# Kernel optimization log

Measured on AMD Instinct MI355X. Metric: run time of the kernel, lower is better.

The kernel has to match this reference:

```python
import jax, jax.numpy as jnp
import numpy as np

N_NODES = 50000
N_EDGES = 600000
D = 128


def _clip(x, c=1.0):
    # per-row L2 clip: x / max(||x|| / c, 1)
    n = jnp.linalg.norm(x, axis=-1, keepdims=True)
    return x / jnp.maximum(n / c, 1.0)


def _priv_sage_conv(x, edge_index, W, b, noise):
    # PrivSAGEConv.forward with perturbation_mode='aggr', root_weight=False
    xc = _clip(x, c=1.0)
    src, dst = edge_index[0], edge_index[1]
    # propagate: gather messages from source nodes, scatter-add at targets
    msg = jax.ops.segment_sum(xc[src], dst, num_segments=x.shape[0])  # [N, D]
    agg = xc + msg + noise  # self term + neighbor sum + DP noise
    return agg @ W.T + b


def setup_inputs() -> dict:
    key = jax.random.key(0)
    ks = jax.random.split(key, 8)
    x = jax.random.normal(ks[0], (N_NODES, D), dtype=jnp.float32)
    edge_index = jax.random.randint(ks[1], (2, N_EDGES), 0, N_NODES, dtype=jnp.int64)
    scale = 1.0 / np.sqrt(D)
    W1 = jax.random.normal(ks[2], (D, D), dtype=jnp.float32) * scale
    b1 = jnp.zeros((D,), dtype=jnp.float32)
    W2 = jax.random.normal(ks[3], (D, D), dtype=jnp.float32) * scale
    b2 = jnp.zeros((D,), dtype=jnp.float32)
    noise1 = jax.random.normal(ks[4], (N_NODES, D), dtype=jnp.float32)
    noise2 = jax.random.normal(ks[5], (N_NODES, D), dtype=jnp.float32)
    return {"x": x, "edge_index": edge_index, "W1": W1, "b1": b1,
            "W2": W2, "b2": b2, "noise1": noise1, "noise2": noise2}


def reference(x, edge_index, W1, b1, W2, b2, noise1, noise2):
    # Layer 1: conv -> (no batchnorm) -> dropout(identity, eval) -> SELU -> stack-combine
    h = _priv_sage_conv(x, edge_index, W1, b1, noise1)
    h = jax.nn.selu(h)
    # Layer 2: last layer, is_pred_module=True -> raw output
    out = _priv_sage_conv(h, edge_index, W2, b2, noise2)
    return out
```

## Files before the change

kernel.cpp:

```cpp
#include <hip/hip_runtime.h>

#define NN 50000
#define NE 600000
#define DD 128
#define NPAD 50048
#define SCAN_BLOCKS 49

typedef __attribute__((ext_vector_type(8))) short bf16x8;
typedef __attribute__((ext_vector_type(4))) float f32x4;

__device__ __forceinline__ float bf2f(unsigned int u16) {
    union { unsigned int i; float f; } v; v.i = u16 << 16; return v.f;
}
__device__ __forceinline__ unsigned short f2bf(float f) {
    union { float f; unsigned int i; } v; v.f = f;
    unsigned int i = v.i + 0x7FFFu + ((v.i >> 16) & 1u);
    return (unsigned short)(i >> 16);
}
__device__ __forceinline__ float wred64(float v) {
    #pragma unroll
    for (int o = 32; o; o >>= 1) v += __shfl_xor(v, o, 64);
    return v;
}
__device__ __forceinline__ int tame16(unsigned int u) {
    int e = (int)((u >> 7) & 0xFF);
    return (e >= 100 && e <= 133) ? 1 : 0;
}

__global__ void probe_k(const int* __restrict__ ei,
                        const unsigned int* __restrict__ xw,
                        const unsigned int* __restrict__ w1w,
                        const unsigned int* __restrict__ nzw,
                        int* __restrict__ flags) {
    const int lane = threadIdx.x;
    int nz = 0;
    #pragma unroll
    for (int i = 0; i < 4; ++i) nz |= ei[2 * (lane * 4 + i) + 1];
    int tx = tame16(xw[lane] & 0xFFFFu);
    int tw = tame16(w1w[lane] & 0xFFFFu);
    int tn = tame16(nzw[lane] & 0xFFFFu);
    #pragma unroll
    for (int o = 32; o; o >>= 1) {
        nz |= __shfl_xor(nz, o, 64);
        tx += __shfl_xor(tx, o, 64);
        tw += __shfl_xor(tw, o, 64);
        tn += __shfl_xor(tn, o, 64);
    }
    if (lane == 0) {
        flags[0] = (nz == 0) ? 1 : 0;
        flags[1] = (tx >= 48) ? 1 : 0;
        flags[2] = (tw >= 48) ? 1 : 0;
        flags[3] = (tn >= 48) ? 1 : 0;
    }
}

__global__ __launch_bounds__(256) void convert_k(
    const void* __restrict__ W1, const void* __restrict__ b1,
    const void* __restrict__ W2, const void* __restrict__ b2,
    const int* __restrict__ flags,
    unsigned short* __restrict__ W1b, unsigned short* __restrict__ b1b,
    unsigned short* __restrict__ W2b, unsigned short* __restrict__ b2b) {
    const int i = blockIdx.x * blockDim.x + threadIdx.x;
    if (i >= DD * DD) return;
    if (flags[2]) {
        W1b[i] = ((const unsigned short*)W1)[i];
        W2b[i] = ((const unsigned short*)W2)[i];
        if (i < DD) { b1b[i] = ((const unsigned short*)b1)[i];
                      b2b[i] = ((const unsigned short*)b2)[i]; }
    } else {
        W1b[i] = f2bf(((const float*)W1)[i]);
        W2b[i] = f2bf(((const float*)W2)[i]);
        if (i < DD) { b1b[i] = f2bf(((const float*)b1)[i]);
                      b2b[i] = f2bf(((const float*)b2)[i]); }
    }
}

__global__ __launch_bounds__(256) void hist_k(
    const int* __restrict__ ei, const int* __restrict__ flags,
    int* __restrict__ deg) {
    const int e = blockIdx.x * blockDim.x + threadIdx.x;
    if (e >= NE) return;
    const int d = flags[0] ? (int)((const long long*)ei)[NE + e] : ei[NE + e];
    atomicAdd(&deg[d], 1);
}

__global__ __launch_bounds__(1024) void scan1_k(
    const int* __restrict__ deg, int* __restrict__ offs,
    int* __restrict__ bsum) {
    __shared__ int wsum[16];
    __shared__ int wbase[16];
    __shared__ int tot_s;
    const int tid = threadIdx.x, lane = tid & 63, wv = tid >> 6;
    const int i = blockIdx.x * 1024 + tid;
    const int v = (i < NN) ? deg[i] : 0;
    int incl = v;
    #pragma unroll
    for (int off = 1; off < 64; off <<= 1) {
        int t = __shfl_up(incl, off, 64);
        if (lane >= off) incl += t;
    }
    if (lane == 63) wsum[wv] = incl;
    __syncthreads();
    if (wv == 0 && lane < 16) {
        const int wv_v = wsum[lane];
        int wincl = wv_v;
        #pragma unroll
        for (int off = 1; off < 16; off <<= 1) {
            int t = __shfl_up(wincl, off, 64);
            if (lane >= off) wincl += t;
        }
        wbase[lane] = wincl - wv_v;
        if (lane == 15) tot_s = wincl;
    }
    __syncthreads();
    if (i < NN) offs[i] = wbase[wv] + incl - v;
    if (tid == 0) bsum[blockIdx.x] = tot_s;
}

__global__ __launch_bounds__(1024) void scan2_k(
    int* __restrict__ offs, int* __restrict__ cursor,
    const int* __restrict__ bsum) {
    __shared__ int base_s;
    const int tid = threadIdx.x;
    if (tid < 64) {
        const int v = (tid < SCAN_BLOCKS) ? bsum[tid] : 0;
        int incl = v;
        #pragma unroll
        for (int off = 1; off < 64; off <<= 1) {
            int t = __shfl_up(incl, off, 64);
            if (tid >= off) incl += t;
        }
        if (tid == blockIdx.x) base_s = incl - v;
    }
    __syncthreads();
    const int i = blockIdx.x * 1024 + tid;
    if (i < NN) {
        const int o = offs[i] + base_s;
        offs[i] = o;
        cursor[i] = o;
    }
    if (blockIdx.x == 0 && tid == 0) offs[NN] = NE;
}

__global__ __launch_bounds__(256) void fill_k(
    const int* __restrict__ ei, const int* __restrict__ flags,
    int* __restrict__ cursor, int* __restrict__ eidx) {
    const int e = blockIdx.x * blockDim.x + threadIdx.x;
    if (e >= NE) return;
    int s, d;
    if (flags[0]) {
        const long long* e64 = (const long long*)ei;
        s = (int)e64[e]; d = (int)e64[NE + e];
    } else {
        s = ei[e]; d = ei[NE + e];
    }
    const int pos = atomicAdd(&cursor[d], 1);
    eidx[pos] = s;
}

__global__ __launch_bounds__(256) void prep_k(
    const void* __restrict__ x, const int* __restrict__ flags,
    unsigned int* __restrict__ featu) {
    const int row = (blockIdx.x * blockDim.x + threadIdx.x) >> 6;
    const int lane = threadIdx.x & 63;
    if (row >= NN) return;
    float v0, v1;
    if (flags[1]) {
        const unsigned int px = ((const unsigned int*)x)[(size_t)row * 64 + lane];
        v0 = bf2f(px & 0xFFFFu); v1 = bf2f(px >> 16);
    } else {
        const float2 px = ((const float2*)x)[(size_t)row * 64 + lane];
        v0 = px.x; v1 = px.y;
    }
    const float ss = wred64(v0 * v0 + v1 * v1);
    const float nrm = sqrtf(ss);
    const float sc = nrm > 1.0f ? 1.0f / nrm : 1.0f;
    featu[(size_t)row * 64 + lane] =
        (unsigned int)f2bf(v0 * sc) | ((unsigned int)f2bf(v1 * sc) << 16);
}

__global__ __launch_bounds__(256) void agg_k(
    const int* __restrict__ offs, const int* __restrict__ eidx,
    const unsigned int* __restrict__ featu, const void* __restrict__ noise,
    const int* __restrict__ flags, unsigned int* __restrict__ aggu) {
    const int node = (blockIdx.x * blockDim.x + threadIdx.x) >> 6;
    const int lane = threadIdx.x & 63;
    if (node >= NN) return;
    const unsigned int u0 = featu[(size_t)node * 64 + lane];
    float ax = bf2f(u0 & 0xFFFFu), ay = bf2f(u0 >> 16);
    if (flags[3]) {
        const unsigned int pn = ((const unsigned int*)noise)[(size_t)node * 64 + lane];
        ax += bf2f(pn & 0xFFFFu); ay += bf2f(pn >> 16);
    } else {
        const float2 n = ((const float2*)noise)[(size_t)node * 64 + lane];
        ax += n.x; ay += n.y;
    }
    const int e1 = offs[node + 1];
    int e = offs[node];
    for (; e + 7 < e1; e += 8) {
        int sidx[8];
        #pragma unroll
        for (int q = 0; q < 8; ++q) sidx[q] = eidx[e + q];
        unsigned int u[8];
        #pragma unroll
        for (int q = 0; q < 8; ++q) u[q] = featu[(size_t)sidx[q] * 64 + lane];
        #pragma unroll
        for (int q = 0; q < 8; ++q) {
            ax += bf2f(u[q] & 0xFFFFu);
            ay += bf2f(u[q] >> 16);
        }
    }
    for (; e < e1; ++e) {
        const unsigned int a = featu[(size_t)eidx[e] * 64 + lane];
        ax += bf2f(a & 0xFFFFu);
        ay += bf2f(a >> 16);
    }
    aggu[(size_t)node * 64 + lane] =
        (unsigned int)f2bf(ax) | ((unsigned int)f2bf(ay) << 16);
}

template<bool LAYER1>
__global__ __launch_bounds__(256) void gemm_k(
    const unsigned short* __restrict__ aggb,
    const unsigned short* __restrict__ Wb,
    const unsigned short* __restrict__ bb,
    unsigned short* __restrict__ featb,
    float* __restrict__ outf) {
    __shared__ unsigned short Wl[128 * 136];
    __shared__ unsigned short bl[128];
    const int t = threadIdx.x;
    #pragma unroll
    for (int i = 0; i < 8; ++i) {
        const int idx8 = t + i * 256;
        const int base = idx8 * 8;
        const int row = base >> 7, col = base & 127;
        *(uint4*)&Wl[row * 136 + col] = ((const uint4*)Wb)[idx8];
    }
    if (t < 128) bl[t] = bb[t];

    const int lane = t & 63;
    const int w = t >> 6;
    const int n15 = lane & 15;
    const int quad = lane >> 4;
    const int rbase = blockIdx.x * 64 + w * 16;

    bf16x8 af[4];
    #pragma unroll
    for (int kc = 0; kc < 4; ++kc)
        af[kc] = *(const bf16x8*)&aggb[(size_t)(rbase + n15) * DD + kc * 32 + quad * 8];

    __syncthreads();

    float h[32];
    #pragma unroll
    for (int nt = 0; nt < 8; ++nt) {
        f32x4 acc = {0.f, 0.f, 0.f, 0.f};
        #pragma unroll
        for (int kc = 0; kc < 4; ++kc) {
            const bf16x8 bfr =
                *(const bf16x8*)&Wl[(nt * 16 + n15) * 136 + kc * 32 + quad * 8];
            acc = __builtin_amdgcn_mfma_f32_16x16x32_bf16(af[kc], bfr, acc, 0, 0, 0);
        }
        const float bj = bf2f((unsigned int)bl[nt * 16 + n15]);
        #pragma unroll
        for (int r = 0; r < 4; ++r) h[nt * 4 + r] = acc[r] + bj;
    }

    if (LAYER1) {
        const float S = 1.0507009873554805f, AL = 1.6732632423543772f;
        float ss[4] = {0.f, 0.f, 0.f, 0.f};
        #pragma unroll
        for (int nt = 0; nt < 8; ++nt)
            #pragma unroll
            for (int r = 0; r < 4; ++r) {
                float v = h[nt * 4 + r];
                v = v > 0.f ? S * v : S * AL * expm1f(v);
                h[nt * 4 + r] = v;
                ss[r] += v * v;
            }
        #pragma unroll
        for (int r = 0; r < 4; ++r) {
            #pragma unroll
            for (int off = 1; off < 16; off <<= 1)
                ss[r] += __shfl_xor(ss[r], off, 64);
        }
        float sc[4];
        #pragma unroll
        for (int r = 0; r < 4; ++r) {
            const float nr = sqrtf(ss[r]);
            sc[r] = nr > 1.f ? 1.f / nr : 1.f;
        }
        #pragma unroll
        for (int r = 0; r < 4; ++r) {
            const int row = rbase + quad * 4 + r;
            if (row < NN) {
                #pragma unroll
                for (int nt = 0; nt < 8; ++nt)
                    featb[(size_t)row * DD + nt * 16 + n15] =
                        f2bf(h[nt * 4 + r] * sc[r]);
            }
        }
    } else {
        #pragma unroll
        for (int r = 0; r < 4; ++r) {
            const int row = rbase + quad * 4 + r;
            if (row < NN) {
                #pragma unroll
                for (int nt = 0; nt < 8; ++nt)
                    outf[(size_t)row * DD + nt * 16 + n15] = h[nt * 4 + r];
            }
        }
    }
}

extern "C" void kernel_launch(void* const* d_in, const int* in_sizes, int n_in,
                              void* d_out, int out_size, void* d_ws, size_t ws_size,
                              hipStream_t stream) {
    const void* x  = d_in[0];
    const int*  ei = (const int*)d_in[1];
    const void* W1 = d_in[2];
    const void* b1 = d_in[3];
    const void* W2 = d_in[4];
    const void* b2 = d_in[5];
    const void* n1 = d_in[6];
    const void* n2 = d_in[7];

    unsigned short* aggb = (unsigned short*)d_ws;
    unsigned short* W1b  = aggb + (size_t)NPAD * DD;
    unsigned short* b1b  = W1b + DD * DD;
    unsigned short* W2b  = b1b + DD;
    unsigned short* b2b  = W2b + DD * DD;
    int* flags  = (int*)(b2b + DD);
    int* deg    = flags + 4;
    int* offs   = deg + NN;
    int* cursor = offs + NN + 1;
    int* bsum   = cursor + NN;
    int* eidx   = bsum + 64;
    unsigned int* featu = (unsigned int*)d_out;

    probe_k<<<1, 64, 0, stream>>>(ei, (const unsigned int*)x,
                                  (const unsigned int*)W1,
                                  (const unsigned int*)n1, flags);
    convert_k<<<(DD * DD + 255) / 256, 256, 0, stream>>>(W1, b1, W2, b2, flags,
                                                         W1b, b1b, W2b, b2b);

    hipMemsetAsync(deg, 0, NN * sizeof(int), stream);
    hist_k<<<(NE + 255) / 256, 256, 0, stream>>>(ei, flags, deg);
    scan1_k<<<SCAN_BLOCKS, 1024, 0, stream>>>(deg, offs, bsum);
    scan2_k<<<SCAN_BLOCKS, 1024, 0, stream>>>(offs, cursor, bsum);
    fill_k<<<(NE + 255) / 256, 256, 0, stream>>>(ei, flags, cursor, eidx);

    prep_k<<<(NN * 64) / 256, 256, 0, stream>>>(x, flags, featu);
    agg_k<<<(NN * 64) / 256, 256, 0, stream>>>(offs, eidx, featu, n1, flags,
                                               (unsigned int*)aggb);
    gemm_k<true><<<NPAD / 64, 256, 0, stream>>>(aggb, W1b, b1b,
                                                (unsigned short*)featu, nullptr);

    agg_k<<<(NN * 64) / 256, 256, 0, stream>>>(offs, eidx, featu, n2, flags,
                                               (unsigned int*)aggb);
    gemm_k<false><<<NPAD / 64, 256, 0, stream>>>(aggb, W2b, b2b, nullptr,
                                                 (float*)d_out);
}
```

Measured before the change: 290.1 us.

## Split aggregation wavefront into half-waves gathering two edges with wider loads

```diff
diff --git a/kernel.cpp b/kernel.cpp
--- a/kernel.cpp
+++ b/kernel.cpp
@@ -163,7 +163,8 @@
     unsigned int* __restrict__ featu) {
     const int row = (blockIdx.x * blockDim.x + threadIdx.x) >> 6;
     const int lane = threadIdx.x & 63;
-    if (row >= NN) return;
+    if (row > NN) return;
+    if (row == NN) { featu[(size_t)NN * 64 + lane] = 0u; return; }
     float v0, v1;
     if (flags[1]) {
         const unsigned int px = ((const unsigned int*)x)[(size_t)row * 64 + lane];
@@ -181,42 +182,64 @@
 
 __global__ __launch_bounds__(256) void agg_k(
     const int* __restrict__ offs, const int* __restrict__ eidx,
-    const unsigned int* __restrict__ featu, const void* __restrict__ noise,
-    const int* __restrict__ flags, unsigned int* __restrict__ aggu) {
+    const uint2* __restrict__ featu2, const void* __restrict__ noise,
+    const int* __restrict__ flags, uint2* __restrict__ aggu2) {
     const int node = (blockIdx.x * blockDim.x + threadIdx.x) >> 6;
     const int lane = threadIdx.x & 63;
     if (node >= NN) return;
-    const unsigned int u0 = featu[(size_t)node * 64 + lane];
-    float ax = bf2f(u0 & 0xFFFFu), ay = bf2f(u0 >> 16);
-    if (flags[3]) {
-        const unsigned int pn = ((const unsigned int*)noise)[(size_t)node * 64 + lane];
-        ax += bf2f(pn & 0xFFFFu); ay += bf2f(pn >> 16);
-    } else {
-        const float2 n = ((const float2*)noise)[(size_t)node * 64 + lane];
-        ax += n.x; ay += n.y;
-    }
-    const int e1 = offs[node + 1];
-    int e = offs[node];
-    for (; e + 7 < e1; e += 8) {
-        int sidx[8];
-        #pragma unroll
-        for (int q = 0; q < 8; ++q) sidx[q] = eidx[e + q];
-        unsigned int u[8];
-        #pragma unroll
-        for (int q = 0; q < 8; ++q) u[q] = featu[(size_t)sidx[q] * 64 + lane];
-        #pragma unroll
-        for (int q = 0; q < 8; ++q) {
-            ax += bf2f(u[q] & 0xFFFFu);
-            ay += bf2f(u[q] >> 16);
-        }
-    }
-    for (; e < e1; ++e) {
-        const unsigned int a = featu[(size_t)eidx[e] * 64 + lane];
-        ax += bf2f(a & 0xFFFFu);
-        ay += bf2f(a >> 16);
-    }
-    aggu[(size_t)node * 64 + lane] =
-        (unsigned int)f2bf(ax) | ((unsigned int)f2bf(ay) << 16);
+    const int c = lane & 31;
+    const int h = lane >> 5;
+
+    float a0, a1, a2, a3;
+    if (h == 0) {
+        const uint2 s = featu2[(size_t)node * 32 + c];
+        a0 = bf2f(s.x & 0xFFFFu); a1 = bf2f(s.x >> 16);
+        a2 = bf2f(s.y & 0xFFFFu); a3 = bf2f(s.y >> 16);
+    } else {
+        if (flags[3]) {
+            const uint2 n = ((const uint2*)noise)[(size_t)node * 32 + c];
+            a0 = bf2f(n.x & 0xFFFFu); a1 = bf2f(n.x >> 16);
+            a2 = bf2f(n.y & 0xFFFFu); a3 = bf2f(n.y >> 16);
+        } else {
+            const float4 n = ((const float4*)noise)[(size_t)node * 32 + c];
+            a0 = n.x; a1 = n.y; a2 = n.z; a3 = n.w;
+        }
+    }
+
+    const int e0 = offs[node];
+    const int cnt = offs[node + 1] - e0;
+    for (int base = 0; base < cnt; base += 64) {
+        const int rem = cnt - base;
+        int myi = NN;
+        if (lane < rem) myi = eidx[e0 + base + lane];
+        const int pairs = (rem < 64 ? rem + 1 : 64) >> 1;
+        const int pb = (pairs + 7) & ~7;
+        for (int p = 0; p < pb; p += 8) {
+            uint2 u[8];
+            #pragma unroll
+            for (int q = 0; q < 8; ++q) {
+                const int s = __shfl(myi, 2 * (p + q) + h, 64);
+                u[q] = featu2[(size_t)s * 32 + c];
+            }
+            #pragma unroll
+            for (int q = 0; q < 8; ++q) {
+                a0 += bf2f(u[q].x & 0xFFFFu); a1 += bf2f(u[q].x >> 16);
+                a2 += bf2f(u[q].y & 0xFFFFu); a3 += bf2f(u[q].y >> 16);
+            }
+        }
+    }
+
+    a0 += __shfl_xor(a0, 32, 64);
+    a1 += __shfl_xor(a1, 32, 64);
+    a2 += __shfl_xor(a2, 32, 64);
+    a3 += __shfl_xor(a3, 32, 64);
+
+    if (h == 0) {
+        uint2 o;
+        o.x = (unsigned int)f2bf(a0) | ((unsigned int)f2bf(a1) << 16);
+        o.y = (unsigned int)f2bf(a2) | ((unsigned int)f2bf(a3) << 16);
+        aggu2[(size_t)node * 32 + c] = o;
+    }
 }
 
 template<bool LAYER1>
@@ -350,14 +373,14 @@
     scan2_k<<<SCAN_BLOCKS, 1024, 0, stream>>>(offs, cursor, bsum);
     fill_k<<<(NE + 255) / 256, 256, 0, stream>>>(ei, flags, cursor, eidx);
 
-    prep_k<<<(NN * 64) / 256, 256, 0, stream>>>(x, flags, featu);
-    agg_k<<<(NN * 64) / 256, 256, 0, stream>>>(offs, eidx, featu, n1, flags,
-                                               (unsigned int*)aggb);
+    prep_k<<<((NN + 1) * 64 + 255) / 256, 256, 0, stream>>>(x, flags, featu);
+    agg_k<<<(NN * 64) / 256, 256, 0, stream>>>(offs, eidx, (const uint2*)featu,
+                                               n1, flags, (uint2*)aggb);
     gemm_k<true><<<NPAD / 64, 256, 0, stream>>>(aggb, W1b, b1b,
                                                 (unsigned short*)featu, nullptr);
 
-    agg_k<<<(NN * 64) / 256, 256, 0, stream>>>(offs, eidx, featu, n2, flags,
-                                               (unsigned int*)aggb);
+    agg_k<<<(NN * 64) / 256, 256, 0, stream>>>(offs, eidx, (const uint2*)featu,
+                                               n2, flags, (uint2*)aggb);
     gemm_k<false><<<NPAD / 64, 256, 0, stream>>>(aggb, W2b, b2b, nullptr,
                                                  (float*)d_out);
 }
```

New measurement: 274.3 us. -5.4%, faster.
